# Performance work log

Measured on AMD Instinct MI355X. Metric: run time of the kernel, lower is better.

The kernel has to match this reference:

```python
import jax, jax.numpy as jnp
import numpy as np

N = 100000
E = 3200000
F_IN = 165
HIDDEN = 16
N_CLASSES = 2


def setup_inputs() -> dict:
    key = jax.random.key(0)
    k1, k2, k3, k4, k5 = jax.random.split(key, 5)
    x = jax.random.normal(k1, (N, F_IN), dtype=jnp.float32)
    edge_index = jax.random.randint(k2, (2, E), 0, N, dtype=jnp.int64)
    # Glorot-style init for GCNConv weights; biases zero (PyG default)
    W1 = jax.random.normal(k3, (F_IN, HIDDEN), dtype=jnp.float32) / np.sqrt(F_IN)
    b1 = jnp.zeros((HIDDEN,), dtype=jnp.float32)
    W2 = jax.random.normal(k4, (HIDDEN, N_CLASSES), dtype=jnp.float32) / np.sqrt(HIDDEN)
    b2 = jnp.zeros((N_CLASSES,), dtype=jnp.float32)
    return {"x": x, "edge_index": edge_index, "W1": W1, "b1": b1, "W2": W2, "b2": b2}


def _gcn_propagate(h, src, dst, dinv_sqrt, num_nodes):
    """Symmetric-normalized aggregation with implicit self-loops.

    out_i = sum_{j->i} dinv[j]*dinv[i]*h_j + dinv[i]^2 * h_i
    """
    norm = (dinv_sqrt[src] * dinv_sqrt[dst])[:, None]          # [E,1]
    msg = h[src] * norm                                        # [E,D] gather
    agg = jax.ops.segment_sum(msg, dst, num_segments=num_nodes)  # [N,D] scatter
    return agg + h * (dinv_sqrt * dinv_sqrt)[:, None]          # self-loop term


def reference(x, edge_index, W1, b1, W2, b2):
    src = edge_index[0]
    dst = edge_index[1]
    n = x.shape[0]
    # degree with self-loops (edge weight 1), as in PyG gcn_norm
    deg = jax.ops.segment_sum(jnp.ones((src.shape[0],), dtype=x.dtype), dst,
                              num_segments=n) + 1.0
    dinv_sqrt = jax.lax.rsqrt(deg)

    # layer 1: transform -> propagate -> bias -> relu
    h = x @ W1                                                 # [N,16]
    h = _gcn_propagate(h, src, dst, dinv_sqrt, n) + b1
    h = jax.nn.relu(h)

    # layer 2
    h = h @ W2                                                 # [N,2]
    h = _gcn_propagate(h, src, dst, dinv_sqrt, n) + b2

    return jax.nn.log_softmax(h, axis=1)
```

## Files before the change

### kernel.cpp

```cpp
#include <hip/hip_runtime.h>
#include <math.h>

#define F_IN 165
#define HID 16
#define NPB 256
#define NPB_BITS 8
#define MAXB 512
#define CHUNK 4096
#define EPT 16
#define SSTAGE 12288

__device__ __forceinline__ unsigned pk_bf16(float lo, float hi) {
    unsigned a = __float_as_uint(lo), b = __float_as_uint(hi);
    a += 0x7FFF + ((a >> 16) & 1);
    b += 0x7FFF + ((b >> 16) & 1);
    return (a >> 16) | (b & 0xFFFF0000u);
}
#define BF_LO(w) __uint_as_float((w) << 16)
#define BF_HI(w) __uint_as_float((w) & 0xFFFF0000u)

__global__ __launch_bounds__(256) void k_cnt(const int* __restrict__ dst,
                                             int* __restrict__ cbM, int E) {
    __shared__ int h[MAXB];
    int t = threadIdx.x;
    for (int i = t; i < MAXB; i += 256) h[i] = 0;
    __syncthreads();
    int e0 = blockIdx.x * CHUNK;
    int n = min(CHUNK, E - e0);
    for (int k = t; k < n; k += 256)
        atomicAdd(&h[dst[e0 + k] >> NPB_BITS], 1);
    __syncthreads();
    for (int i = t; i < MAXB; i += 256)
        cbM[blockIdx.x * MAXB + i] = h[i];
}

__global__ __launch_bounds__(256) void k_colscan(int* __restrict__ cbM,
                                                 int* __restrict__ btot, int NB) {
    __shared__ int ps[256];
    int b = blockIdx.x, t = threadIdx.x;
    int i0 = t * 4;
    int v[4];
    int s = 0;
#pragma unroll
    for (int u = 0; u < 4; ++u) {
        int c = i0 + u;
        v[u] = (c < NB) ? cbM[c * MAXB + b] : 0;
        s += v[u];
    }
    ps[t] = s;
    __syncthreads();
    for (int off = 1; off < 256; off <<= 1) {
        int a = (t >= off) ? ps[t - off] : 0;
        __syncthreads();
        ps[t] += a;
        __syncthreads();
    }
    int run = ps[t] - s;
#pragma unroll
    for (int u = 0; u < 4; ++u) {
        int c = i0 + u;
        if (c < NB) cbM[c * MAXB + b] = run;
        run += v[u];
    }
    if (t == 255) btot[b] = ps[255];
}

__global__ __launch_bounds__(256) void k_bscan(const int* __restrict__ btot,
                                               int* __restrict__ bofs,
                                               int* __restrict__ rowptr,
                                               int nbuck, int N) {
    __shared__ int ps[256];
    int t = threadIdx.x;
    int i0 = 2 * t, i1 = 2 * t + 1;
    int c0 = (i0 < nbuck) ? btot[i0] : 0;
    int c1 = (i1 < nbuck) ? btot[i1] : 0;
    int s = c0 + c1;
    ps[t] = s;
    __syncthreads();
    for (int off = 1; off < 256; off <<= 1) {
        int a = (t >= off) ? ps[t - off] : 0;
        __syncthreads();
        ps[t] += a;
        __syncthreads();
    }
    int excl = ps[t] - s;
    if (i0 < nbuck) bofs[i0] = excl;
    if (i1 < nbuck) bofs[i1] = excl + c0;
    if (t == 255) { bofs[nbuck] = ps[255]; rowptr[N] = ps[255]; }
}

__global__ __launch_bounds__(256) void k_binscatter(const int* __restrict__ src,
                                                    const int* __restrict__ dst,
                                                    const int* __restrict__ cbM,
                                                    const int* __restrict__ bofs,
                                                    unsigned* __restrict__ sedge,
                                                    int E, int nbuck) {
    __shared__ int hist[MAXB];
    __shared__ int lofs[MAXB];
    __shared__ int dlt[MAXB];
    __shared__ int ps[256];
    __shared__ uint2 stg[CHUNK];
    int t = threadIdx.x;
    int me = blockIdx.x;
    int e0 = me * CHUNK;
    int n = min(CHUNK, E - e0);

    int d[EPT], sv[EPT], rk[EPT];
#pragma unroll
    for (int u = 0; u < EPT; ++u) {
        int k = t + u * 256;
        d[u]  = (k < n) ? dst[e0 + k] : -1;
        sv[u] = (k < n) ? src[e0 + k] : 0;
    }
    for (int i = t; i < MAXB; i += 256) hist[i] = 0;
    __syncthreads();
#pragma unroll
    for (int u = 0; u < EPT; ++u)
        if (d[u] >= 0) rk[u] = atomicAdd(&hist[d[u] >> NPB_BITS], 1);
    __syncthreads();

    int base = t * 2;
    int h0 = hist[base], h1 = hist[base + 1];
    int s = h0 + h1;
    ps[t] = s;
    __syncthreads();
    for (int off = 1; off < 256; off <<= 1) {
        int a = (t >= off) ? ps[t - off] : 0;
        __syncthreads();
        ps[t] += a;
        __syncthreads();
    }
    int excl = ps[t] - s;
    lofs[base] = excl;
    lofs[base + 1] = excl + h0;
    __syncthreads();
    for (int i = t; i < nbuck; i += 256)
        dlt[i] = bofs[i] + cbM[me * MAXB + i] - lofs[i];
    __syncthreads();

#pragma unroll
    for (int u = 0; u < EPT; ++u) {
        if (d[u] < 0) continue;
        int b = d[u] >> NPB_BITS;
        int r = lofs[b] + rk[u];
        stg[r] = make_uint2(((unsigned)sv[u] << NPB_BITS) | (unsigned)(d[u] & (NPB - 1)),
                            (unsigned)(dlt[b] + r));
    }
    __syncthreads();

    for (int r = t; r < n; r += 256) {
        uint2 v = stg[r];
        sedge[v.y] = v.x;
    }
}

__global__ __launch_bounds__(256) void k_sortnode(const int* __restrict__ bofs,
                                                  const unsigned* __restrict__ sedge,
                                                  int* __restrict__ csr,
                                                  int* __restrict__ rowptr,
                                                  float* __restrict__ dinv, int N) {
    __shared__ int hist[256];
    __shared__ int ps[256];
    __shared__ int lcur[256];
    __shared__ int stage[SSTAGE];
    int b = blockIdx.x, t = threadIdx.x;
    int base = bofs[b];
    int n = bofs[b + 1] - base;
    hist[t] = 0;
    __syncthreads();
    for (int k = t; k < n; k += 256)
        atomicAdd(&hist[sedge[base + k] & (NPB - 1)], 1);
    __syncthreads();
    int c = hist[t];
    ps[t] = c;
    __syncthreads();
    for (int off = 1; off < 256; off <<= 1) {
        int a = (t >= off) ? ps[t - off] : 0;
        __syncthreads();
        ps[t] += a;
        __syncthreads();
    }
    int excl = ps[t] - c;
    int node = b * NPB + t;
    if (node < N) {
        rowptr[node] = base + excl;
        dinv[node] = rsqrtf((float)c + 1.0f);
    }
    lcur[t] = excl;
    __syncthreads();
    bool staged = (n <= SSTAGE);
    for (int k = t; k < n; k += 256) {
        unsigned p = sedge[base + k];
        int d = p & (NPB - 1);
        int pos = atomicAdd(&lcur[d], 1);
        int sv = (int)(p >> NPB_BITS);
        if (staged) stage[pos] = sv;
        else        csr[base + pos] = sv;
    }
    __syncthreads();
    if (staged) {
        for (int k = t; k < n; k += 256) csr[base + k] = stage[k];
    }
}

#define FMA1(vv, kk)                                                   \
    {                                                                  \
        float4 w = *(const float4*)(ws + (kk) * HID + c4);             \
        acc.x = fmaf((vv), w.x, acc.x); acc.y = fmaf((vv), w.y, acc.y);\
        acc.z = fmaf((vv), w.z, acc.z); acc.w = fmaf((vv), w.w, acc.w);\
    }

__global__ __launch_bounds__(256) void k_gemm1(const float* __restrict__ x,
                                               const float* __restrict__ W1,
                                               const float* __restrict__ dinv,
                                               unsigned* __restrict__ g1, int N) {
    __shared__ float ws[F_IN * HID];
    int t = threadIdx.x;
    {
        const float4* w4 = (const float4*)W1;
        float4* s4 = (float4*)ws;
#pragma unroll
        for (int u = 0; u < 3; ++u) {
            int i = t + u * 256;
            if (i < (F_IN * HID) / 4) s4[i] = w4[i];
        }
    }
    __syncthreads();
    int gid = blockIdx.x * 256 + t;
    int row = gid >> 2;
    int c4 = (gid & 3) << 2;
    if (row >= N) return;
    const float* xr = x + (long long)row * F_IN;
    float4 acc = make_float4(0.f, 0.f, 0.f, 0.f);

    int p = (4 - (row & 3)) & 3;
    for (int k = 0; k < p; ++k) { float v = xr[k]; FMA1(v, k); }

    const float4* xr4 = (const float4*)(xr + p);
    int n4 = (F_IN - p) >> 2;
    int q = 0;
    for (; q + 4 <= n4; q += 4) {
        float4 v0 = xr4[q], v1 = xr4[q + 1], v2 = xr4[q + 2], v3 = xr4[q + 3];
        int kb = p + q * 4;
        FMA1(v0.x, kb + 0)  FMA1(v0.y, kb + 1)  FMA1(v0.z, kb + 2)  FMA1(v0.w, kb + 3)
        FMA1(v1.x, kb + 4)  FMA1(v1.y, kb + 5)  FMA1(v1.z, kb + 6)  FMA1(v1.w, kb + 7)
        FMA1(v2.x, kb + 8)  FMA1(v2.y, kb + 9)  FMA1(v2.z, kb + 10) FMA1(v2.w, kb + 11)
        FMA1(v3.x, kb + 12) FMA1(v3.y, kb + 13) FMA1(v3.z, kb + 14) FMA1(v3.w, kb + 15)
    }
    for (; q < n4; ++q) {
        float4 v = xr4[q];
        int kb = p + q * 4;
        FMA1(v.x, kb) FMA1(v.y, kb + 1) FMA1(v.z, kb + 2) FMA1(v.w, kb + 3)
    }
    for (int k = p + n4 * 4; k < F_IN; ++k) { float v = xr[k]; FMA1(v, k); }

    float di = dinv[row];
    uint2 o = make_uint2(pk_bf16(acc.x * di, acc.y * di),
                         pk_bf16(acc.z * di, acc.w * di));
    *(uint2*)(g1 + (long long)row * 8 + (gid & 3) * 2) = o;
}

__global__ __launch_bounds__(256) void k_agg1(const int* __restrict__ rowptr,
                                              const int* __restrict__ csr,
                                              const unsigned* __restrict__ g1,
                                              const float* __restrict__ dinv,
                                              const float* __restrict__ b1,
                                              const float* __restrict__ W2,
                                              float* __restrict__ g2, int N) {
    int gid = blockIdx.x * 256 + threadIdx.x;
    int i = gid >> 3;
    int j = gid & 7;
    if (i >= N) return;
    int e0 = rowptr[i], e1 = rowptr[i + 1];
    unsigned w0 = g1[i * 8 + j];
    float a0 = BF_LO(w0), a1 = BF_HI(w0);
    int e = e0;
    for (; e + 8 <= e1; e += 8) {
        int s0 = csr[e],     s1 = csr[e + 1], s2 = csr[e + 2], s3 = csr[e + 3];
        int s4 = csr[e + 4], s5 = csr[e + 5], s6 = csr[e + 6], s7 = csr[e + 7];
        unsigned u0 = g1[s0 * 8 + j], u1 = g1[s1 * 8 + j];
        unsigned u2 = g1[s2 * 8 + j], u3 = g1[s3 * 8 + j];
        unsigned u4 = g1[s4 * 8 + j], u5 = g1[s5 * 8 + j];
        unsigned u6 = g1[s6 * 8 + j], u7 = g1[s7 * 8 + j];
        a0 += ((BF_LO(u0) + BF_LO(u1)) + (BF_LO(u2) + BF_LO(u3))) +
              ((BF_LO(u4) + BF_LO(u5)) + (BF_LO(u6) + BF_LO(u7)));
        a1 += ((BF_HI(u0) + BF_HI(u1)) + (BF_HI(u2) + BF_HI(u3))) +
              ((BF_HI(u4) + BF_HI(u5)) + (BF_HI(u6) + BF_HI(u7)));
    }
    for (; e < e1; ++e) {
        unsigned u = g1[csr[e] * 8 + j];
        a0 += BF_LO(u);
        a1 += BF_HI(u);
    }
    float di = dinv[i];
    float v0 = fmaf(a0, di, b1[2 * j]);     v0 = v0 > 0.f ? v0 : 0.f;
    float v1 = fmaf(a1, di, b1[2 * j + 1]); v1 = v1 > 0.f ? v1 : 0.f;
    float4 w = ((const float4*)W2)[j];
    float c0 = fmaf(v1, w.z, v0 * w.x);
    float c1 = fmaf(v1, w.w, v0 * w.y);
    for (int off = 4; off; off >>= 1) {
        c0 += __shfl_xor(c0, off, 8);
        c1 += __shfl_xor(c1, off, 8);
    }
    if (j == 0) ((float2*)g2)[i] = make_float2(c0 * di, c1 * di);
}

__global__ __launch_bounds__(256) void k_agg2(const int* __restrict__ rowptr,
                                              const int* __restrict__ csr,
                                              const float* __restrict__ g2,
                                              const float* __restrict__ dinv,
                                              const float* __restrict__ b2,
                                              float* __restrict__ out, int N) {
    int gid = blockIdx.x * 256 + threadIdx.x;
    int i = gid >> 2;
    int l = gid & 3;
    if (i >= N) return;
    int e0 = rowptr[i], e1 = rowptr[i + 1];
    float a0 = 0.f, a1 = 0.f;
    int e = e0 + l;
    for (; e + 4 < e1; e += 8) {
        int s0 = csr[e], s1 = csr[e + 4];
        float2 u = ((const float2*)g2)[s0];
        float2 w = ((const float2*)g2)[s1];
        a0 += u.x + w.x;
        a1 += u.y + w.y;
    }
    for (; e < e1; e += 4) {
        int s = csr[e];
        float2 u = ((const float2*)g2)[s];
        a0 += u.x;
        a1 += u.y;
    }
    a0 += __shfl_xor(a0, 1, 4); a0 += __shfl_xor(a0, 2, 4);
    a1 += __shfl_xor(a1, 1, 4); a1 += __shfl_xor(a1, 2, 4);
    if (l == 0) {
        float2 self = ((const float2*)g2)[i];
        float di = dinv[i];
        float A = fmaf(a0 + self.x, di, b2[0]);
        float B = fmaf(a1 + self.y, di, b2[1]);
        float m = fmaxf(A, B);
        float lse = m + logf(expf(A - m) + expf(B - m));
        ((float2*)out)[i] = make_float2(A - lse, B - lse);
    }
}

extern "C" void kernel_launch(void* const* d_in, const int* in_sizes, int n_in,
                              void* d_out, int out_size, void* d_ws, size_t ws_size,
                              hipStream_t stream) {
    const float* x  = (const float*)d_in[0];
    const int*   ei = (const int*)d_in[1];
    const float* W1 = (const float*)d_in[2];
    const float* b1 = (const float*)d_in[3];
    const float* W2 = (const float*)d_in[4];
    const float* b2 = (const float*)d_in[5];
    float* out = (float*)d_out;

    int N = in_sizes[0] / F_IN;
    int E = in_sizes[1] / 2;
    const int* src = ei;
    const int* dst = ei + E;
    int nbuck = (N + NPB - 1) >> NPB_BITS;
    int NB = (E + CHUNK - 1) / CHUNK;

    int* cbM      = (int*)d_ws;
    int* btot     = cbM + (long long)NB * MAXB;
    int* bofs     = btot + MAXB;
    int* rowptr   = bofs + MAXB + 1;
    unsigned* sedge = (unsigned*)(rowptr + N + 1);
    int* csr      = (int*)(sedge + E);
    float* dinv   = (float*)(csr + E);
    unsigned* g1  = (unsigned*)(dinv + N);
    float* g2     = (float*)(g1 + (long long)8 * N);

    k_cnt<<<NB, 256, 0, stream>>>(dst, cbM, E);
    k_colscan<<<nbuck, 256, 0, stream>>>(cbM, btot, NB);
    k_bscan<<<1, 256, 0, stream>>>(btot, bofs, rowptr, nbuck, N);
    k_binscatter<<<NB, 256, 0, stream>>>(src, dst, cbM, bofs, sedge, E, nbuck);
    k_sortnode<<<nbuck, 256, 0, stream>>>(bofs, sedge, csr, rowptr, dinv, N);

    k_gemm1<<<(N * 4 + 255) / 256, 256, 0, stream>>>(x, W1, dinv, g1, N);

    k_agg1<<<(N * 8 + 255) / 256, 256, 0, stream>>>(rowptr, csr, g1, dinv, b1, W2, g2, N);
    k_agg2<<<(N * 4 + 255) / 256, 256, 0, stream>>>(rowptr, csr, g2, dinv, b2, out, N);
}
```

Measured before the change: 128.1 us.

## Compute full 16-wide output row per thread in gemm1, read W1 from global

The first-layer GEMM now has one thread compute all 16 hidden outputs of a row, instead of four threads each computing 4 columns. This cuts the redundant reads of x from four per row to one, and each thread writes its whole bf16 row with two 16-byte stores. W1 is now read from global memory through the wave-uniform scalar/constant path instead of being staged in shared memory. The cost is more registers and less per-row parallelism, and with 64-thread blocks each thread's strided loads of x may coalesce poorly.

```diff
diff --git a/kernel.cpp b/kernel.cpp
--- a/kernel.cpp
+++ b/kernel.cpp
@@ -203,61 +203,51 @@
     }
 }
 
-#define FMA1(vv, kk)                                                   \
-    {                                                                  \
-        float4 w = *(const float4*)(ws + (kk) * HID + c4);             \
-        acc.x = fmaf((vv), w.x, acc.x); acc.y = fmaf((vv), w.y, acc.y);\
-        acc.z = fmaf((vv), w.z, acc.z); acc.w = fmaf((vv), w.w, acc.w);\
-    }
-
-__global__ __launch_bounds__(256) void k_gemm1(const float* __restrict__ x,
-                                               const float* __restrict__ W1,
-                                               const float* __restrict__ dinv,
-                                               unsigned* __restrict__ g1, int N) {
-    __shared__ float ws[F_IN * HID];
-    int t = threadIdx.x;
-    {
-        const float4* w4 = (const float4*)W1;
-        float4* s4 = (float4*)ws;
-#pragma unroll
-        for (int u = 0; u < 3; ++u) {
-            int i = t + u * 256;
-            if (i < (F_IN * HID) / 4) s4[i] = w4[i];
-        }
-    }
-    __syncthreads();
-    int gid = blockIdx.x * 256 + t;
-    int row = gid >> 2;
-    int c4 = (gid & 3) << 2;
+#define FMAROW(vv, kk)                                                  \
+    {                                                                   \
+        const float* w = W1 + (kk) * HID;                               \
+        _Pragma("unroll")                                               \
+        for (int c = 0; c < HID; ++c) acc[c] = fmaf((vv), w[c], acc[c]);\
+    }
+
+__global__ __launch_bounds__(64) void k_gemm1(const float* __restrict__ x,
+                                              const float* __restrict__ W1,
+                                              const float* __restrict__ dinv,
+                                              unsigned* __restrict__ g1, int N) {
+    int row = blockIdx.x * 64 + threadIdx.x;
     if (row >= N) return;
     const float* xr = x + (long long)row * F_IN;
-    float4 acc = make_float4(0.f, 0.f, 0.f, 0.f);
+    float acc[HID];
+#pragma unroll
+    for (int c = 0; c < HID; ++c) acc[c] = 0.f;
 
     int p = (4 - (row & 3)) & 3;
-    for (int k = 0; k < p; ++k) { float v = xr[k]; FMA1(v, k); }
+    for (int k = 0; k < p; ++k) { float v = xr[k]; FMAROW(v, k); }
 
     const float4* xr4 = (const float4*)(xr + p);
     int n4 = (F_IN - p) >> 2;
-    int q = 0;
-    for (; q + 4 <= n4; q += 4) {
-        float4 v0 = xr4[q], v1 = xr4[q + 1], v2 = xr4[q + 2], v3 = xr4[q + 3];
-        int kb = p + q * 4;
-        FMA1(v0.x, kb + 0)  FMA1(v0.y, kb + 1)  FMA1(v0.z, kb + 2)  FMA1(v0.w, kb + 3)
-        FMA1(v1.x, kb + 4)  FMA1(v1.y, kb + 5)  FMA1(v1.z, kb + 6)  FMA1(v1.w, kb + 7)
-        FMA1(v2.x, kb + 8)  FMA1(v2.y, kb + 9)  FMA1(v2.z, kb + 10) FMA1(v2.w, kb + 11)
-        FMA1(v3.x, kb + 12) FMA1(v3.y, kb + 13) FMA1(v3.z, kb + 14) FMA1(v3.w, kb + 15)
-    }
-    for (; q < n4; ++q) {
+    for (int q = 0; q < n4; ++q) {
         float4 v = xr4[q];
         int kb = p + q * 4;
-        FMA1(v.x, kb) FMA1(v.y, kb + 1) FMA1(v.z, kb + 2) FMA1(v.w, kb + 3)
-    }
-    for (int k = p + n4 * 4; k < F_IN; ++k) { float v = xr[k]; FMA1(v, k); }
+        FMAROW(v.x, kb + 0)
+        FMAROW(v.y, kb + 1)
+        FMAROW(v.z, kb + 2)
+        FMAROW(v.w, kb + 3)
+    }
+    for (int k = p + n4 * 4; k < F_IN; ++k) { float v = xr[k]; FMAROW(v, k); }
 
     float di = dinv[row];
-    uint2 o = make_uint2(pk_bf16(acc.x * di, acc.y * di),
-                         pk_bf16(acc.z * di, acc.w * di));
-    *(uint2*)(g1 + (long long)row * 8 + (gid & 3) * 2) = o;
+    unsigned* o = g1 + (long long)row * 8;
+    uint4 o0 = make_uint4(pk_bf16(acc[0] * di, acc[1] * di),
+                          pk_bf16(acc[2] * di, acc[3] * di),
+                          pk_bf16(acc[4] * di, acc[5] * di),
+                          pk_bf16(acc[6] * di, acc[7] * di));
+    uint4 o1 = make_uint4(pk_bf16(acc[8] * di, acc[9] * di),
+                          pk_bf16(acc[10] * di, acc[11] * di),
+                          pk_bf16(acc[12] * di, acc[13] * di),
+                          pk_bf16(acc[14] * di, acc[15] * di));
+    *(uint4*)(o)     = o0;
+    *(uint4*)(o + 4) = o1;
 }
 
 __global__ __launch_bounds__(256) void k_agg1(const int* __restrict__ rowptr,
@@ -378,7 +368,7 @@
     k_binscatter<<<NB, 256, 0, stream>>>(src, dst, cbM, bofs, sedge, E, nbuck);
     k_sortnode<<<nbuck, 256, 0, stream>>>(bofs, sedge, csr, rowptr, dinv, N);
 
-    k_gemm1<<<(N * 4 + 255) / 256, 256, 0, stream>>>(x, W1, dinv, g1, N);
+    k_gemm1<<<(N + 63) / 64, 64, 0, stream>>>(x, W1, dinv, g1, N);
 
     k_agg1<<<(N * 8 + 255) / 256, 256, 0, stream>>>(rowptr, csr, g1, dinv, b1, W2, g2, N);
     k_agg2<<<(N * 4 + 255) / 256, 256, 0, stream>>>(rowptr, csr, g2, dinv, b2, out, N);
```

After: 176.7 us. +37.9%, slower.

## Fuse bucket scan into consumers, vectorize edge loads, widen agg1 gathers to uint4

Applied to the files above, without the earlier changes.

Removes the single-block bucket-offset scan kernel and recomputes the 512-entry prefix scan redundantly inside each binscatter and sortnode block, saving one launch and a serial dependency. Edge-index loads in the count and binscatter kernels use int4 when the chunk is full. The first aggregation switches from 8 threads per node with 32-bit gathers to 2 threads per node with 128-bit gathers, handling 8 features per thread. The cost is redundant scan work per block and fewer threads in flight for the gather, which lowers memory-level parallelism on the latency-bound aggregation.

```diff
diff --git a/kernel.cpp b/kernel.cpp
--- a/kernel.cpp
+++ b/kernel.cpp
@@ -27,8 +27,20 @@
     __syncthreads();
     int e0 = blockIdx.x * CHUNK;
     int n = min(CHUNK, E - e0);
-    for (int k = t; k < n; k += 256)
-        atomicAdd(&h[dst[e0 + k] >> NPB_BITS], 1);
+    if (n == CHUNK) {
+        const int4* d4 = (const int4*)(dst + e0);
+#pragma unroll
+        for (int u = 0; u < 4; ++u) {
+            int4 v = d4[u * 256 + t];
+            atomicAdd(&h[v.x >> NPB_BITS], 1);
+            atomicAdd(&h[v.y >> NPB_BITS], 1);
+            atomicAdd(&h[v.z >> NPB_BITS], 1);
+            atomicAdd(&h[v.w >> NPB_BITS], 1);
+        }
+    } else {
+        for (int k = t; k < n; k += 256)
+            atomicAdd(&h[dst[e0 + k] >> NPB_BITS], 1);
+    }
     __syncthreads();
     for (int i = t; i < MAXB; i += 256)
         cbM[blockIdx.x * MAXB + i] = h[i];
@@ -65,34 +77,10 @@
     if (t == 255) btot[b] = ps[255];
 }
 
-__global__ __launch_bounds__(256) void k_bscan(const int* __restrict__ btot,
-                                               int* __restrict__ bofs,
-                                               int* __restrict__ rowptr,
-                                               int nbuck, int N) {
-    __shared__ int ps[256];
-    int t = threadIdx.x;
-    int i0 = 2 * t, i1 = 2 * t + 1;
-    int c0 = (i0 < nbuck) ? btot[i0] : 0;
-    int c1 = (i1 < nbuck) ? btot[i1] : 0;
-    int s = c0 + c1;
-    ps[t] = s;
-    __syncthreads();
-    for (int off = 1; off < 256; off <<= 1) {
-        int a = (t >= off) ? ps[t - off] : 0;
-        __syncthreads();
-        ps[t] += a;
-        __syncthreads();
-    }
-    int excl = ps[t] - s;
-    if (i0 < nbuck) bofs[i0] = excl;
-    if (i1 < nbuck) bofs[i1] = excl + c0;
-    if (t == 255) { bofs[nbuck] = ps[255]; rowptr[N] = ps[255]; }
-}
-
 __global__ __launch_bounds__(256) void k_binscatter(const int* __restrict__ src,
                                                     const int* __restrict__ dst,
                                                     const int* __restrict__ cbM,
-                                                    const int* __restrict__ bofs,
+                                                    const int* __restrict__ btot,
                                                     unsigned* __restrict__ sedge,
                                                     int E, int nbuck) {
     __shared__ int hist[MAXB];
@@ -106,11 +94,25 @@
     int n = min(CHUNK, E - e0);
 
     int d[EPT], sv[EPT], rk[EPT];
-#pragma unroll
-    for (int u = 0; u < EPT; ++u) {
-        int k = t + u * 256;
-        d[u]  = (k < n) ? dst[e0 + k] : -1;
-        sv[u] = (k < n) ? src[e0 + k] : 0;
+    if (n == CHUNK) {
+        const int4* dd = (const int4*)(dst + e0);
+        const int4* ss = (const int4*)(src + e0);
+#pragma unroll
+        for (int u = 0; u < 4; ++u) {
+            int4 dv = dd[u * 256 + t];
+            int4 vv = ss[u * 256 + t];
+            d[u * 4 + 0] = dv.x; d[u * 4 + 1] = dv.y;
+            d[u * 4 + 2] = dv.z; d[u * 4 + 3] = dv.w;
+            sv[u * 4 + 0] = vv.x; sv[u * 4 + 1] = vv.y;
+            sv[u * 4 + 2] = vv.z; sv[u * 4 + 3] = vv.w;
+        }
+    } else {
+#pragma unroll
+        for (int u = 0; u < EPT; ++u) {
+            int k = t + u * 256;
+            d[u]  = (k < n) ? dst[e0 + k] : -1;
+            sv[u] = (k < n) ? src[e0 + k] : 0;
+        }
     }
     for (int i = t; i < MAXB; i += 256) hist[i] = 0;
     __syncthreads();
@@ -133,9 +135,25 @@
     int excl = ps[t] - s;
     lofs[base] = excl;
     lofs[base + 1] = excl + h0;
+
+    int c0v = (base < nbuck) ? btot[base] : 0;
+    int c1v = (base + 1 < nbuck) ? btot[base + 1] : 0;
+    int s2 = c0v + c1v;
+    __syncthreads();
+    ps[t] = s2;
+    __syncthreads();
+    for (int off = 1; off < 256; off <<= 1) {
+        int a = (t >= off) ? ps[t - off] : 0;
+        __syncthreads();
+        ps[t] += a;
+        __syncthreads();
+    }
+    int ex2 = ps[t] - s2;
+    hist[base] = ex2;
+    hist[base + 1] = ex2 + c0v;
     __syncthreads();
     for (int i = t; i < nbuck; i += 256)
-        dlt[i] = bofs[i] + cbM[me * MAXB + i] - lofs[i];
+        dlt[i] = hist[i] + cbM[me * MAXB + i] - lofs[i];
     __syncthreads();
 
 #pragma unroll
@@ -154,18 +172,37 @@
     }
 }
 
-__global__ __launch_bounds__(256) void k_sortnode(const int* __restrict__ bofs,
+__global__ __launch_bounds__(256) void k_sortnode(const int* __restrict__ btot,
                                                   const unsigned* __restrict__ sedge,
                                                   int* __restrict__ csr,
                                                   int* __restrict__ rowptr,
-                                                  float* __restrict__ dinv, int N) {
+                                                  float* __restrict__ dinv,
+                                                  int nbuck, int N) {
     __shared__ int hist[256];
     __shared__ int ps[256];
     __shared__ int lcur[256];
     __shared__ int stage[SSTAGE];
+    __shared__ int sbase;
     int b = blockIdx.x, t = threadIdx.x;
-    int base = bofs[b];
-    int n = bofs[b + 1] - base;
+
+    int t2 = 2 * t;
+    int c0v = (t2 < nbuck) ? btot[t2] : 0;
+    int c1v = (t2 + 1 < nbuck) ? btot[t2 + 1] : 0;
+    int ssum = c0v + c1v;
+    ps[t] = ssum;
+    __syncthreads();
+    for (int off = 1; off < 256; off <<= 1) {
+        int a = (t >= off) ? ps[t - off] : 0;
+        __syncthreads();
+        ps[t] += a;
+        __syncthreads();
+    }
+    if (t == (b >> 1)) sbase = (ps[t] - ssum) + ((b & 1) ? c0v : 0);
+    __syncthreads();
+    int base = sbase;
+    int n = btot[b];
+    if (b == nbuck - 1 && t == 0) rowptr[N] = base + n;
+
     hist[t] = 0;
     __syncthreads();
     for (int k = t; k < n; k += 256)
@@ -191,11 +228,11 @@
     bool staged = (n <= SSTAGE);
     for (int k = t; k < n; k += 256) {
         unsigned p = sedge[base + k];
-        int d = p & (NPB - 1);
-        int pos = atomicAdd(&lcur[d], 1);
-        int sv = (int)(p >> NPB_BITS);
-        if (staged) stage[pos] = sv;
-        else        csr[base + pos] = sv;
+        int dd = p & (NPB - 1);
+        int pos = atomicAdd(&lcur[dd], 1);
+        int svv = (int)(p >> NPB_BITS);
+        if (staged) stage[pos] = svv;
+        else        csr[base + pos] = svv;
     }
     __syncthreads();
     if (staged) {
@@ -260,6 +297,10 @@
     *(uint2*)(g1 + (long long)row * 8 + (gid & 3) * 2) = o;
 }
 
+#define ACC8(U)                                                         \
+    l0 += BF_LO(U.x); h0 += BF_HI(U.x); l1 += BF_LO(U.y); h1 += BF_HI(U.y); \
+    l2 += BF_LO(U.z); h2 += BF_HI(U.z); l3 += BF_LO(U.w); h3 += BF_HI(U.w);
+
 __global__ __launch_bounds__(256) void k_agg1(const int* __restrict__ rowptr,
                                               const int* __restrict__ csr,
                                               const unsigned* __restrict__ g1,
@@ -268,40 +309,40 @@
                                               const float* __restrict__ W2,
                                               float* __restrict__ g2, int N) {
     int gid = blockIdx.x * 256 + threadIdx.x;
-    int i = gid >> 3;
-    int j = gid & 7;
+    int i = gid >> 1;
+    int j = gid & 1;
     if (i >= N) return;
     int e0 = rowptr[i], e1 = rowptr[i + 1];
-    unsigned w0 = g1[i * 8 + j];
-    float a0 = BF_LO(w0), a1 = BF_HI(w0);
+    const uint4* G = (const uint4*)g1;
+    uint4 w0 = G[i * 2 + j];
+    float l0 = BF_LO(w0.x), h0 = BF_HI(w0.x), l1 = BF_LO(w0.y), h1 = BF_HI(w0.y);
+    float l2 = BF_LO(w0.z), h2 = BF_HI(w0.z), l3 = BF_LO(w0.w), h3 = BF_HI(w0.w);
     int e = e0;
-    for (; e + 8 <= e1; e += 8) {
-        int s0 = csr[e],     s1 = csr[e + 1], s2 = csr[e + 2], s3 = csr[e + 3];
-        int s4 = csr[e + 4], s5 = csr[e + 5], s6 = csr[e + 6], s7 = csr[e + 7];
-        unsigned u0 = g1[s0 * 8 + j], u1 = g1[s1 * 8 + j];
-        unsigned u2 = g1[s2 * 8 + j], u3 = g1[s3 * 8 + j];
-        unsigned u4 = g1[s4 * 8 + j], u5 = g1[s5 * 8 + j];
-        unsigned u6 = g1[s6 * 8 + j], u7 = g1[s7 * 8 + j];
-        a0 += ((BF_LO(u0) + BF_LO(u1)) + (BF_LO(u2) + BF_LO(u3))) +
-              ((BF_LO(u4) + BF_LO(u5)) + (BF_LO(u6) + BF_LO(u7)));
-        a1 += ((BF_HI(u0) + BF_HI(u1)) + (BF_HI(u2) + BF_HI(u3))) +
-              ((BF_HI(u4) + BF_HI(u5)) + (BF_HI(u6) + BF_HI(u7)));
+    for (; e + 4 <= e1; e += 4) {
+        int s0 = csr[e], s1 = csr[e + 1], s2 = csr[e + 2], s3 = csr[e + 3];
+        uint4 u0 = G[s0 * 2 + j], u1 = G[s1 * 2 + j];
+        uint4 u2 = G[s2 * 2 + j], u3 = G[s3 * 2 + j];
+        ACC8(u0) ACC8(u1) ACC8(u2) ACC8(u3)
     }
     for (; e < e1; ++e) {
-        unsigned u = g1[csr[e] * 8 + j];
-        a0 += BF_LO(u);
-        a1 += BF_HI(u);
+        uint4 u = G[csr[e] * 2 + j];
+        ACC8(u)
     }
     float di = dinv[i];
-    float v0 = fmaf(a0, di, b1[2 * j]);     v0 = v0 > 0.f ? v0 : 0.f;
-    float v1 = fmaf(a1, di, b1[2 * j + 1]); v1 = v1 > 0.f ? v1 : 0.f;
-    float4 w = ((const float4*)W2)[j];
-    float c0 = fmaf(v1, w.z, v0 * w.x);
-    float c1 = fmaf(v1, w.w, v0 * w.y);
-    for (int off = 4; off; off >>= 1) {
-        c0 += __shfl_xor(c0, off, 8);
-        c1 += __shfl_xor(c1, off, 8);
-    }
+    int fb = j * 8;
+    float c0 = 0.f, c1 = 0.f;
+#define EPI(val, fi)                                                     \
+    {                                                                    \
+        float v = fmaf((val), di, b1[fb + (fi)]);                        \
+        v = v > 0.f ? v : 0.f;                                           \
+        float2 w = ((const float2*)W2)[fb + (fi)];                       \
+        c0 = fmaf(v, w.x, c0);                                           \
+        c1 = fmaf(v, w.y, c1);                                           \
+    }
+    EPI(l0, 0) EPI(h0, 1) EPI(l1, 2) EPI(h1, 3)
+    EPI(l2, 4) EPI(h2, 5) EPI(l3, 6) EPI(h3, 7)
+    c0 += __shfl_xor(c0, 1, 2);
+    c1 += __shfl_xor(c1, 1, 2);
     if (j == 0) ((float2*)g2)[i] = make_float2(c0 * di, c1 * di);
 }
 
@@ -364,8 +405,7 @@
 
     int* cbM      = (int*)d_ws;
     int* btot     = cbM + (long long)NB * MAXB;
-    int* bofs     = btot + MAXB;
-    int* rowptr   = bofs + MAXB + 1;
+    int* rowptr   = btot + MAXB;
     unsigned* sedge = (unsigned*)(rowptr + N + 1);
     int* csr      = (int*)(sedge + E);
     float* dinv   = (float*)(csr + E);
@@ -374,12 +414,11 @@
 
     k_cnt<<<NB, 256, 0, stream>>>(dst, cbM, E);
     k_colscan<<<nbuck, 256, 0, stream>>>(cbM, btot, NB);
-    k_bscan<<<1, 256, 0, stream>>>(btot, bofs, rowptr, nbuck, N);
-    k_binscatter<<<NB, 256, 0, stream>>>(src, dst, cbM, bofs, sedge, E, nbuck);
-    k_sortnode<<<nbuck, 256, 0, stream>>>(bofs, sedge, csr, rowptr, dinv, N);
+    k_binscatter<<<NB, 256, 0, stream>>>(src, dst, cbM, btot, sedge, E, nbuck);
+    k_sortnode<<<nbuck, 256, 0, stream>>>(btot, sedge, csr, rowptr, dinv, nbuck, N);
 
     k_gemm1<<<(N * 4 + 255) / 256, 256, 0, stream>>>(x, W1, dinv, g1, N);
 
-    k_agg1<<<(N * 8 + 255) / 256, 256, 0, stream>>>(rowptr, csr, g1, dinv, b1, W2, g2, N);
+    k_agg1<<<(N * 2 + 255) / 256, 256, 0, stream>>>(rowptr, csr, g1, dinv, b1, W2, g2, N);
     k_agg2<<<(N * 4 + 255) / 256, 256, 0, stream>>>(rowptr, csr, g2, dinv, b2, out, N);
 }
```

Measured after the change: 131.4 us. 1.03x slower.
